# Kernel optimization log

Hardware: AMD Instinct MI355X
Metric: run time of the kernel (lower is better)

## Reference

```python
import jax, jax.numpy as jnp
import numpy as np

D_MODEL = 2048
NUM_HEADS = 16
D_K = 128
SEQ_LEN = 4096
BATCH = 4


def make_rope(max_seq_len, d, dtype=jnp.float32):
    # theta_i = 1/10000^(2i/d), pos_enc = outer(pos, theta), buffer = [sin | cos] along last dim -> [S, d]
    theta = 1.0 / jnp.power(10000.0, jnp.arange(0, d, 2, dtype=dtype) / d)
    pos = jnp.arange(max_seq_len, dtype=dtype)
    pe = pos[:, None] * theta[None, :]                     # [S, d/2]
    return jnp.concatenate([jnp.sin(pe), jnp.cos(pe)], axis=-1)  # [S, d]


def apply_rope(x, rope):
    # x: [..., S, d_k], rope: [S, d_k] (already sliced to S)
    d_k = x.shape[-1]
    scale = jnp.sqrt(jnp.asarray(d_k, dtype=x.dtype))
    x = x * scale
    x1, x2 = x[..., ::2], x[..., 1::2]
    r1, r2 = rope[..., ::2], rope[..., 1::2]
    return jnp.concatenate([x1 * r1 - x2 * r2, x2 * r1 + x1 * r2], axis=-1)


def setup_inputs() -> dict:
    key = jax.random.key(0)
    ks = jax.random.split(key, 7)
    sq = 1.0 / np.sqrt(D_MODEL)
    x = jax.random.normal(ks[0], (BATCH, SEQ_LEN, D_MODEL), dtype=jnp.float32)
    Wq = jax.random.uniform(ks[1], (D_MODEL, NUM_HEADS * D_K), jnp.float32, -sq, sq)
    bq = jax.random.uniform(ks[2], (NUM_HEADS * D_K,), jnp.float32, -sq, sq)
    Wk = jax.random.uniform(ks[3], (D_MODEL, D_K), jnp.float32, -sq, sq)
    bk = jax.random.uniform(ks[4], (D_K,), jnp.float32, -sq, sq)
    Wv = jax.random.uniform(ks[5], (D_MODEL, D_K), jnp.float32, -sq, sq)
    bv = jax.random.uniform(ks[6], (D_K,), jnp.float32, -sq, sq)
    return {"x": x, "Wq": Wq, "bq": bq, "Wk": Wk, "bk": bk, "Wv": Wv, "bv": bv}


def reference(x, Wq, bq, Wk, bk, Wv, bv):
    B, S, _ = x.shape
    rope = make_rope(SEQ_LEN, D_K, x.dtype)[:S]            # [S, d_k]
    Q = (jnp.einsum('bsd,de->bse', x, Wq) + bq)            # [B, S, H*d_k]
    Q = Q.reshape(B, S, NUM_HEADS, D_K).transpose(0, 2, 1, 3)  # [B, H, S, d_k]
    Q = apply_rope(Q, rope)
    K = apply_rope(jnp.einsum('bsd,de->bse', x, Wk) + bk, rope)  # [B, S, d_k]
    V = apply_rope(jnp.einsum('bsd,de->bse', x, Wv) + bv, rope)  # [B, S, d_k]
    return (Q, K, V)
```

## Files before the change

kernel.cpp:

```cpp
#include <hip/hip_runtime.h>
#include <hip/hip_bf16.h>
#include <math.h>

#define D_MODEL 2048
#define NUM_HEADS 16
#define D_K 128
#define SEQ_LEN 4096
#define BATCH 4
#define M_ROWS 16384
#define N_TOT 2304
#define KT 32

#define XB_BYTES 67108864ull
#define WT_BYTES 9437184ull
#define BP_BYTES 16384ull

typedef __attribute__((ext_vector_type(8))) short bf16x8;
typedef __attribute__((ext_vector_type(8))) unsigned short u16x8;
typedef __attribute__((ext_vector_type(4))) float f32x4;

__device__ __forceinline__ unsigned short f2bf(float f) {
  unsigned int u = __builtin_bit_cast(unsigned int, f);
  u += 0x7fffu + ((u >> 16) & 1u);
  return (unsigned short)(u >> 16);
}

__device__ __forceinline__ void async16(const unsigned char* g, unsigned char* l) {
  __builtin_amdgcn_global_load_lds(
      (const __attribute__((address_space(1))) void*)g,
      (__attribute__((address_space(3))) void*)l, 16, 0, 0);
}

__global__ void rope_kernel(float* __restrict__ ropeT) {
  int idx = blockIdx.x * 256 + threadIdx.x;
  int o = idx & 63;
  int sp = idx >> 6;
  int j1 = (o < 32) ? (2 * o) : (2 * (o - 32));
  float th1 = 1.0f / powf(10000.0f, (float)j1 / 64.0f);
  float th2 = 1.0f / powf(10000.0f, (float)(j1 + 1) / 64.0f);
  float a1 = (float)sp * th1;
  float a2 = (float)sp * th2;
  float v1 = (o < 32) ? sinf(a1) : cosf(a1);
  float v2 = (o < 32) ? sinf(a2) : cosf(a2);
  const float sc = 11.3137084989847604f;
  ropeT[sp * 128 + o]      = v1 * sc;
  ropeT[sp * 128 + 64 + o] = v2 * sc;
}

__global__ void bias_kernel(const float* __restrict__ bq, const float* __restrict__ bk,
                            const float* __restrict__ bv, float* __restrict__ bp) {
  int n = blockIdx.x * 256 + threadIdx.x;
  if (n >= N_TOT) return;
  int r = n & 127, nb = n >> 7;
  int d = (r < 64) ? (2 * r) : (2 * (r - 64) + 1);
  float v;
  if (nb < 16)       v = bq[nb * 128 + d];
  else if (nb == 16) v = bk[d];
  else               v = bv[d];
  bp[n] = v;
}

__global__ void wsplit_kernel(const float* __restrict__ Wq, const float* __restrict__ Wk,
                              const float* __restrict__ Wv, unsigned char* __restrict__ wt) {
  int R = threadIdx.x;
  int c   = blockIdx.x & 7;
  int kt  = (blockIdx.x >> 3) & 31;
  int nb2 = blockIdx.x >> 8;
  int wng = R >> 6, q = R & 63, a = q >> 4, lr = q & 15;
  int s = wng >> 1, w = wng & 1;
  int tq = 2 * w + (a & 1) + 4 * (a >> 1);
  int col = tq * 16 + lr;
  int d = (col < 64) ? (2 * col) : (2 * (col - 64) + 1);
  int n = (nb2 * 2 + s) * 128 + d;
  const float* src; int ld, cc;
  if (n < 2048)      { src = Wq; ld = 2048; cc = n; }
  else if (n < 2176) { src = Wk; ld = 128;  cc = n - 2048; }
  else               { src = Wv; ld = 128;  cc = n - 2176; }
  int k0 = kt * 64 + c * 8;
  u16x8 H;
#pragma unroll
  for (int j = 0; j < 8; j++) H[j] = f2bf(src[(size_t)(k0 + j) * ld + cc]);
  unsigned char* tile = wt + (((size_t)(nb2 * 32 + kt)) << 15);
  *(u16x8*)(tile + R * 128 + ((c ^ (R & 7)) << 4)) = H;
}

__global__ void xcast_kernel(const float* __restrict__ x, unsigned char* __restrict__ xb) {
  int idx = blockIdx.x * 256 + threadIdx.x;
  int c  = idx & 7;
  int r  = (idx >> 3) & 255;
  int kt = (idx >> 11) & 31;
  int mb = idx >> 16;
  const float4* p = (const float4*)(x + ((size_t)(mb * 256 + r)) * D_MODEL + kt * 64 + c * 8);
  float4 v0 = p[0], v1 = p[1];
  float v[8] = {v0.x, v0.y, v0.z, v0.w, v1.x, v1.y, v1.z, v1.w};
  u16x8 H;
#pragma unroll
  for (int j = 0; j < 8; j++) H[j] = f2bf(v[j]);
  unsigned char* tile = xb + (((size_t)(mb * 32 + kt)) << 15);
  *(u16x8*)(tile + r * 128 + ((c ^ (r & 7)) << 4)) = H;
}

__global__ __launch_bounds__(512, 2)
void gemm_rope_kernel(const unsigned char* __restrict__ xb,
                      const unsigned char* __restrict__ wt,
                      const float* __restrict__ bp,
                      const float* __restrict__ ropeT,
                      float* __restrict__ out) {
  __shared__ __align__(16) unsigned char lds[131072];

  const int tid = threadIdx.x;
  const int wave = tid >> 6, lane = tid & 63;
  const int lr = lane & 15, gl = lane >> 4;
  const int wm = wave >> 2;
  const int wng = wave & 3;

  int bid = blockIdx.x;
  int wg = (bid & 7) * 72 + (bid >> 3);
  const int mb  = wg / 9;
  const int nb2 = wg % 9;

  const int sw = lr & 7;
  int aoff[8], boff[4];
#pragma unroll
  for (int i = 0; i < 8; i++)
    aoff[i] = (wm * 128 + i * 16 + lr) * 128 + ((gl ^ sw) << 4);
#pragma unroll
  for (int a = 0; a < 4; a++)
    boff[a] = 32768 + (wng * 64 + a * 16 + lr) * 128 + ((gl ^ sw) << 4);

  f32x4 acc[8][4];
#pragma unroll
  for (int i = 0; i < 8; i++)
#pragma unroll
    for (int a = 0; a < 4; a++) acc[i][a] = (f32x4){0.f, 0.f, 0.f, 0.f};

  const unsigned char* gA = xb + ((size_t)(mb * KT) << 15);
  const unsigned char* gB = wt + ((size_t)(nb2 * KT) << 15);
  const int aro = wm * 16384 + wng * 1024;
  const int bro = wng * 8192 + wm * 4096;

#pragma unroll
  for (int j = 0; j < 4; j++)
    async16(gB + bro + j * 1024 + lane * 16, lds + 32768 + bro + j * 1024);
#pragma unroll
  for (int j = 0; j < 4; j++)
    async16(gA + aro + j * 4096 + lane * 16, lds + aro + j * 4096);
  asm volatile("s_waitcnt vmcnt(3)" ::: "memory");
  __builtin_amdgcn_s_barrier();
  __builtin_amdgcn_sched_barrier(0);

#define PHASE_BODY(p, CS, STAGE, K)                                                        \
  {                                                                                        \
    bf16x8 x0h = *(const bf16x8*)(lds + (CS) + aoff[2*(p)]);                               \
    bf16x8 x0l = *(const bf16x8*)(lds + (CS) + (aoff[2*(p)] ^ 64));                        \
    bf16x8 x1h = *(const bf16x8*)(lds + (CS) + aoff[2*(p)+1]);                             \
    bf16x8 x1l = *(const bf16x8*)(lds + (CS) + (aoff[2*(p)+1] ^ 64));                      \
    STAGE                                                                                  \
    __builtin_amdgcn_s_setprio(1);                                                         \
    _Pragma("unroll")                                                                      \
    for (int a_ = 0; a_ < 4; ++a_) {                                                       \
      acc[2*(p)][a_]   = __builtin_amdgcn_mfma_f32_16x16x32_bf16(x0h, bh[a_], acc[2*(p)][a_], 0,0,0);   \
      acc[2*(p)][a_]   = __builtin_amdgcn_mfma_f32_16x16x32_bf16(x0l, bl[a_], acc[2*(p)][a_], 0,0,0);   \
      acc[2*(p)+1][a_] = __builtin_amdgcn_mfma_f32_16x16x32_bf16(x1h, bh[a_], acc[2*(p)+1][a_], 0,0,0); \
      acc[2*(p)+1][a_] = __builtin_amdgcn_mfma_f32_16x16x32_bf16(x1l, bl[a_], acc[2*(p)+1][a_], 0,0,0); \
    }                                                                                      \
    __builtin_amdgcn_s_setprio(0);                                                         \
    asm volatile("s_waitcnt vmcnt(" K ")" ::: "memory");                                   \
    __builtin_amdgcn_s_barrier();                                                          \
    __builtin_amdgcn_sched_barrier(0);                                                     \
  }

#define STAGE_B01 { async16(gBn + bro + lane*16, lB + bro);                 \
                    async16(gBn + bro + 1024 + lane*16, lB + bro + 1024); }
#define STAGE_B23 { async16(gBn + bro + 2048 + lane*16, lB + bro + 2048);   \
                    async16(gBn + bro + 3072 + lane*16, lB + bro + 3072); }
#define STAGE_A01 { async16(gAn + aro + lane*16, lA + aro);                 \
                    async16(gAn + aro + 4096 + lane*16, lA + aro + 4096); }
#define STAGE_A23 { async16(gAn + aro + 8192 + lane*16, lA + aro + 8192);   \
                    async16(gAn + aro + 12288 + lane*16, lA + aro + 12288); }
#define STAGE_NONE {}

  for (int t = 0; t < KT - 1; ++t) {
    const int CS = (t & 1) << 16;
    unsigned char* lA = lds + (CS ^ 65536);
    unsigned char* lB = lA + 32768;
    const unsigned char* gAn = gA + ((size_t)(t + 1) << 15);
    const unsigned char* gBn = gB + ((size_t)(t + 1) << 15);
    bf16x8 bh[4], bl[4];
#pragma unroll
    for (int a = 0; a < 4; a++) {
      bh[a] = *(const bf16x8*)(lds + CS + boff[a]);
      bl[a] = *(const bf16x8*)(lds + CS + (boff[a] ^ 64));
    }
    PHASE_BODY(0, CS, STAGE_B01, "4")
    PHASE_BODY(1, CS, STAGE_B23, "5")
    PHASE_BODY(2, CS, STAGE_A01, "6")
    PHASE_BODY(3, CS, STAGE_A23, "3")
  }
  {
    const int CS = ((KT - 1) & 1) << 16;
    bf16x8 bh[4], bl[4];
#pragma unroll
    for (int a = 0; a < 4; a++) {
      bh[a] = *(const bf16x8*)(lds + CS + boff[a]);
      bl[a] = *(const bf16x8*)(lds + CS + (boff[a] ^ 64));
    }
    PHASE_BODY(0, CS, STAGE_NONE, "2")
    PHASE_BODY(1, CS, STAGE_NONE, "1")
    PHASE_BODY(2, CS, STAGE_NONE, "0")
    PHASE_BODY(3, CS, STAGE_NONE, "0")
  }
#undef PHASE_BODY
#undef STAGE_B01
#undef STAGE_B23
#undef STAGE_A01
#undef STAGE_A23
#undef STAGE_NONE

  const int m0 = mb * 256 + wm * 128;
  const int ssub = wng >> 1, w = wng & 1;
  const int nbv = nb2 * 2 + ssub;
#pragma unroll
  for (int i = 0; i < 8; i++) {
#pragma unroll
    for (int a = 0; a < 2; a++) {
      int op = (2 * w + a) * 16 + lr;
      int nlo = nbv * 128 + op;
      float blo = bp[nlo], bhi = bp[nlo + 64];
#pragma unroll
      for (int r = 0; r < 4; r++) {
        int row = m0 + i * 16 + gl * 4 + r;
        int sp = row & (SEQ_LEN - 1);
        int b = row >> 12;
        float t1 = acc[i][a][r]     + blo;
        float t2 = acc[i][a + 2][r] + bhi;
        float R1 = ropeT[sp * 128 + op];
        float R2 = ropeT[sp * 128 + 64 + op];
        float olo = R1 * t1 - R2 * t2;
        float ohi = R2 * t1 + R1 * t2;
        size_t base;
        if (nbv < 16)       base = (((size_t)(b * NUM_HEADS + nbv)) * SEQ_LEN + sp) * D_K;
        else if (nbv == 16) base = (size_t)M_ROWS * D_MODEL
                                   + ((size_t)(b * SEQ_LEN + sp)) * D_K;
        else                base = (size_t)M_ROWS * D_MODEL + (size_t)M_ROWS * D_K
                                   + ((size_t)(b * SEQ_LEN + sp)) * D_K;
        out[base + op]      = olo;
        out[base + op + 64] = ohi;
      }
    }
  }
}

extern "C" void kernel_launch(void* const* d_in, const int* in_sizes, int n_in,
                              void* d_out, int out_size, void* d_ws, size_t ws_size,
                              hipStream_t stream) {
  const float* x  = (const float*)d_in[0];
  const float* Wq = (const float*)d_in[1];
  const float* bq = (const float*)d_in[2];
  const float* Wk = (const float*)d_in[3];
  const float* bk = (const float*)d_in[4];
  const float* Wv = (const float*)d_in[5];
  const float* bv = (const float*)d_in[6];
  float* out = (float*)d_out;

  unsigned char* ws = (unsigned char*)d_ws;
  unsigned char* xb = ws;
  unsigned char* wt = ws + XB_BYTES;
  float* bp    = (float*)(ws + XB_BYTES + WT_BYTES);
  float* ropeT = (float*)(ws + XB_BYTES + WT_BYTES + BP_BYTES);

  rope_kernel<<<1024, 256, 0, stream>>>(ropeT);
  bias_kernel<<<9, 256, 0, stream>>>(bq, bk, bv, bp);
  wsplit_kernel<<<2304, 256, 0, stream>>>(Wq, Wk, Wv, wt);
  xcast_kernel<<<16384, 256, 0, stream>>>(x, xb);
  gemm_rope_kernel<<<576, 512, 0, stream>>>(xb, wt, bp, ropeT, out);
}
```

Measured before the change: 446.2 us.

## Switch GEMM to 32x32x16 MFMA tiles with simpler per-K-step double buffering

Replaces the 16x16x32 MFMA inner loop with 32x32x16 bf16 MFMAs, rearranging the weight pre-pack layout, the LDS fragment offsets and the epilogue row mapping to match. The fine-grained four-phase staged prefetch with partial vmcnt waits is replaced by issuing the whole next K-tile at the start of each iteration, followed by one full wait and barrier. Larger MFMA tiles cut the number of LDS fragment reads and MFMA issues per FLOP. The coarser synchronization may expose more load latency than the previous interleaved schedule.

```diff
diff --git a/kernel.cpp b/kernel.cpp
--- a/kernel.cpp
+++ b/kernel.cpp
@@ -17,7 +17,7 @@
 
 typedef __attribute__((ext_vector_type(8))) short bf16x8;
 typedef __attribute__((ext_vector_type(8))) unsigned short u16x8;
-typedef __attribute__((ext_vector_type(4))) float f32x4;
+typedef __attribute__((ext_vector_type(16))) float f32x16;
 
 __device__ __forceinline__ unsigned short f2bf(float f) {
   unsigned int u = __builtin_bit_cast(unsigned int, f);
@@ -66,11 +66,10 @@
   int c   = blockIdx.x & 7;
   int kt  = (blockIdx.x >> 3) & 31;
   int nb2 = blockIdx.x >> 8;
-  int wng = R >> 6, q = R & 63, a = q >> 4, lr = q & 15;
-  int s = wng >> 1, w = wng & 1;
-  int tq = 2 * w + (a & 1) + 4 * (a >> 1);
-  int col = tq * 16 + lr;
-  int d = (col < 64) ? (2 * col) : (2 * (col - 64) + 1);
+  int wng = R >> 6, j = (R >> 5) & 1, c31 = R & 31;
+  int opfull = (wng & 1) * 32 + j * 64 + c31;
+  int s = wng >> 1;
+  int d = (opfull < 64) ? (2 * opfull) : (2 * (opfull - 64) + 1);
   int n = (nb2 * 2 + s) * 128 + d;
   const float* src; int ld, cc;
   if (n < 2048)      { src = Wq; ld = 2048; cc = n; }
@@ -79,7 +78,7 @@
   int k0 = kt * 64 + c * 8;
   u16x8 H;
 #pragma unroll
-  for (int j = 0; j < 8; j++) H[j] = f2bf(src[(size_t)(k0 + j) * ld + cc]);
+  for (int jj = 0; jj < 8; jj++) H[jj] = f2bf(src[(size_t)(k0 + jj) * ld + cc]);
   unsigned char* tile = wt + (((size_t)(nb2 * 32 + kt)) << 15);
   *(u16x8*)(tile + R * 128 + ((c ^ (R & 7)) << 4)) = H;
 }
@@ -95,7 +94,7 @@
   float v[8] = {v0.x, v0.y, v0.z, v0.w, v1.x, v1.y, v1.z, v1.w};
   u16x8 H;
 #pragma unroll
-  for (int j = 0; j < 8; j++) H[j] = f2bf(v[j]);
+  for (int jj = 0; jj < 8; jj++) H[jj] = f2bf(v[jj]);
   unsigned char* tile = xb + (((size_t)(mb * 32 + kt)) << 15);
   *(u16x8*)(tile + r * 128 + ((c ^ (r & 7)) << 4)) = H;
 }
@@ -110,7 +109,7 @@
 
   const int tid = threadIdx.x;
   const int wave = tid >> 6, lane = tid & 63;
-  const int lr = lane & 15, gl = lane >> 4;
+  const int c31 = lane & 31, h = lane >> 5;
   const int wm = wave >> 2;
   const int wng = wave & 3;
 
@@ -119,134 +118,111 @@
   const int mb  = wg / 9;
   const int nb2 = wg % 9;
 
-  const int sw = lr & 7;
-  int aoff[8], boff[4];
-#pragma unroll
-  for (int i = 0; i < 8; i++)
-    aoff[i] = (wm * 128 + i * 16 + lr) * 128 + ((gl ^ sw) << 4);
-#pragma unroll
-  for (int a = 0; a < 4; a++)
-    boff[a] = 32768 + (wng * 64 + a * 16 + lr) * 128 + ((gl ^ sw) << 4);
-
-  f32x4 acc[8][4];
-#pragma unroll
-  for (int i = 0; i < 8; i++)
-#pragma unroll
-    for (int a = 0; a < 4; a++) acc[i][a] = (f32x4){0.f, 0.f, 0.f, 0.f};
+  int aoff[4][4], boff[2][4];
+#pragma unroll
+  for (int i = 0; i < 4; i++) {
+    int row = wm * 128 + i * 32 + c31;
+#pragma unroll
+    for (int q = 0; q < 4; q++)
+      aoff[i][q] = row * 128 + (((2 * q + h) ^ (row & 7)) << 4);
+  }
+#pragma unroll
+  for (int j = 0; j < 2; j++) {
+    int rowb = wng * 64 + j * 32 + c31;
+#pragma unroll
+    for (int q = 0; q < 4; q++)
+      boff[j][q] = 32768 + rowb * 128 + (((2 * q + h) ^ (rowb & 7)) << 4);
+  }
+
+  f32x16 acc[4][2];
+#pragma unroll
+  for (int i = 0; i < 4; i++)
+#pragma unroll
+    for (int j = 0; j < 2; j++)
+#pragma unroll
+      for (int r = 0; r < 16; r++) acc[i][j][r] = 0.f;
 
   const unsigned char* gA = xb + ((size_t)(mb * KT) << 15);
   const unsigned char* gB = wt + ((size_t)(nb2 * KT) << 15);
   const int aro = wm * 16384 + wng * 1024;
   const int bro = wng * 8192 + wm * 4096;
 
-#pragma unroll
-  for (int j = 0; j < 4; j++)
-    async16(gB + bro + j * 1024 + lane * 16, lds + 32768 + bro + j * 1024);
-#pragma unroll
-  for (int j = 0; j < 4; j++)
-    async16(gA + aro + j * 4096 + lane * 16, lds + aro + j * 4096);
-  asm volatile("s_waitcnt vmcnt(3)" ::: "memory");
+#define ISSUE(tt)                                                              \
+  do {                                                                         \
+    const unsigned char* gA_ = gA + ((size_t)(tt) << 15) + aro + lane * 16;    \
+    const unsigned char* gB_ = gB + ((size_t)(tt) << 15) + bro + lane * 16;    \
+    unsigned char* lA_ = lds + (((tt) & 1) << 16) + aro;                       \
+    unsigned char* lB_ = lds + (((tt) & 1) << 16) + 32768 + bro;               \
+    async16(gA_,         lA_);                                                 \
+    async16(gA_ + 4096,  lA_ + 4096);                                          \
+    async16(gA_ + 8192,  lA_ + 8192);                                          \
+    async16(gA_ + 12288, lA_ + 12288);                                         \
+    async16(gB_,         lB_);                                                 \
+    async16(gB_ + 1024,  lB_ + 1024);                                          \
+    async16(gB_ + 2048,  lB_ + 2048);                                          \
+    async16(gB_ + 3072,  lB_ + 3072);                                          \
+  } while (0)
+
+  ISSUE(0);
+  asm volatile("s_waitcnt vmcnt(0)" ::: "memory");
   __builtin_amdgcn_s_barrier();
   __builtin_amdgcn_sched_barrier(0);
 
-#define PHASE_BODY(p, CS, STAGE, K)                                                        \
-  {                                                                                        \
-    bf16x8 x0h = *(const bf16x8*)(lds + (CS) + aoff[2*(p)]);                               \
-    bf16x8 x0l = *(const bf16x8*)(lds + (CS) + (aoff[2*(p)] ^ 64));                        \
-    bf16x8 x1h = *(const bf16x8*)(lds + (CS) + aoff[2*(p)+1]);                             \
-    bf16x8 x1l = *(const bf16x8*)(lds + (CS) + (aoff[2*(p)+1] ^ 64));                      \
-    STAGE                                                                                  \
-    __builtin_amdgcn_s_setprio(1);                                                         \
-    _Pragma("unroll")                                                                      \
-    for (int a_ = 0; a_ < 4; ++a_) {                                                       \
-      acc[2*(p)][a_]   = __builtin_amdgcn_mfma_f32_16x16x32_bf16(x0h, bh[a_], acc[2*(p)][a_], 0,0,0);   \
-      acc[2*(p)][a_]   = __builtin_amdgcn_mfma_f32_16x16x32_bf16(x0l, bl[a_], acc[2*(p)][a_], 0,0,0);   \
-      acc[2*(p)+1][a_] = __builtin_amdgcn_mfma_f32_16x16x32_bf16(x1h, bh[a_], acc[2*(p)+1][a_], 0,0,0); \
-      acc[2*(p)+1][a_] = __builtin_amdgcn_mfma_f32_16x16x32_bf16(x1l, bl[a_], acc[2*(p)+1][a_], 0,0,0); \
-    }                                                                                      \
-    __builtin_amdgcn_s_setprio(0);                                                         \
-    asm volatile("s_waitcnt vmcnt(" K ")" ::: "memory");                                   \
-    __builtin_amdgcn_s_barrier();                                                          \
-    __builtin_amdgcn_sched_barrier(0);                                                     \
-  }
-
-#define STAGE_B01 { async16(gBn + bro + lane*16, lB + bro);                 \
-                    async16(gBn + bro + 1024 + lane*16, lB + bro + 1024); }
-#define STAGE_B23 { async16(gBn + bro + 2048 + lane*16, lB + bro + 2048);   \
-                    async16(gBn + bro + 3072 + lane*16, lB + bro + 3072); }
-#define STAGE_A01 { async16(gAn + aro + lane*16, lA + aro);                 \
-                    async16(gAn + aro + 4096 + lane*16, lA + aro + 4096); }
-#define STAGE_A23 { async16(gAn + aro + 8192 + lane*16, lA + aro + 8192);   \
-                    async16(gAn + aro + 12288 + lane*16, lA + aro + 12288); }
-#define STAGE_NONE {}
-
-  for (int t = 0; t < KT - 1; ++t) {
-    const int CS = (t & 1) << 16;
-    unsigned char* lA = lds + (CS ^ 65536);
-    unsigned char* lB = lA + 32768;
-    const unsigned char* gAn = gA + ((size_t)(t + 1) << 15);
-    const unsigned char* gBn = gB + ((size_t)(t + 1) << 15);
-    bf16x8 bh[4], bl[4];
-#pragma unroll
-    for (int a = 0; a < 4; a++) {
-      bh[a] = *(const bf16x8*)(lds + CS + boff[a]);
-      bl[a] = *(const bf16x8*)(lds + CS + (boff[a] ^ 64));
+  for (int t = 0; t < KT; ++t) {
+    if (t + 1 < KT) ISSUE(t + 1);
+    const unsigned char* sl = lds + ((t & 1) << 16);
+#pragma unroll
+    for (int q = 0; q < 4; ++q) {
+      bf16x8 A0 = *(const bf16x8*)(sl + aoff[0][q]);
+      bf16x8 A1 = *(const bf16x8*)(sl + aoff[1][q]);
+      bf16x8 A2 = *(const bf16x8*)(sl + aoff[2][q]);
+      bf16x8 A3 = *(const bf16x8*)(sl + aoff[3][q]);
+      bf16x8 B0 = *(const bf16x8*)(sl + boff[0][q]);
+      bf16x8 B1 = *(const bf16x8*)(sl + boff[1][q]);
+      __builtin_amdgcn_s_setprio(1);
+      acc[0][0] = __builtin_amdgcn_mfma_f32_32x32x16_bf16(A0, B0, acc[0][0], 0, 0, 0);
+      acc[0][1] = __builtin_amdgcn_mfma_f32_32x32x16_bf16(A0, B1, acc[0][1], 0, 0, 0);
+      acc[1][0] = __builtin_amdgcn_mfma_f32_32x32x16_bf16(A1, B0, acc[1][0], 0, 0, 0);
+      acc[1][1] = __builtin_amdgcn_mfma_f32_32x32x16_bf16(A1, B1, acc[1][1], 0, 0, 0);
+      acc[2][0] = __builtin_amdgcn_mfma_f32_32x32x16_bf16(A2, B0, acc[2][0], 0, 0, 0);
+      acc[2][1] = __builtin_amdgcn_mfma_f32_32x32x16_bf16(A2, B1, acc[2][1], 0, 0, 0);
+      acc[3][0] = __builtin_amdgcn_mfma_f32_32x32x16_bf16(A3, B0, acc[3][0], 0, 0, 0);
+      acc[3][1] = __builtin_amdgcn_mfma_f32_32x32x16_bf16(A3, B1, acc[3][1], 0, 0, 0);
+      __builtin_amdgcn_s_setprio(0);
     }
-    PHASE_BODY(0, CS, STAGE_B01, "4")
-    PHASE_BODY(1, CS, STAGE_B23, "5")
-    PHASE_BODY(2, CS, STAGE_A01, "6")
-    PHASE_BODY(3, CS, STAGE_A23, "3")
-  }
-  {
-    const int CS = ((KT - 1) & 1) << 16;
-    bf16x8 bh[4], bl[4];
-#pragma unroll
-    for (int a = 0; a < 4; a++) {
-      bh[a] = *(const bf16x8*)(lds + CS + boff[a]);
-      bl[a] = *(const bf16x8*)(lds + CS + (boff[a] ^ 64));
-    }
-    PHASE_BODY(0, CS, STAGE_NONE, "2")
-    PHASE_BODY(1, CS, STAGE_NONE, "1")
-    PHASE_BODY(2, CS, STAGE_NONE, "0")
-    PHASE_BODY(3, CS, STAGE_NONE, "0")
-  }
-#undef PHASE_BODY
-#undef STAGE_B01
-#undef STAGE_B23
-#undef STAGE_A01
-#undef STAGE_A23
-#undef STAGE_NONE
+    __builtin_amdgcn_sched_barrier(0);
+    asm volatile("s_waitcnt vmcnt(0)" ::: "memory");
+    __builtin_amdgcn_s_barrier();
+    __builtin_amdgcn_sched_barrier(0);
+  }
+#undef ISSUE
 
   const int m0 = mb * 256 + wm * 128;
-  const int ssub = wng >> 1, w = wng & 1;
-  const int nbv = nb2 * 2 + ssub;
-#pragma unroll
-  for (int i = 0; i < 8; i++) {
-#pragma unroll
-    for (int a = 0; a < 2; a++) {
-      int op = (2 * w + a) * 16 + lr;
-      int nlo = nbv * 128 + op;
-      float blo = bp[nlo], bhi = bp[nlo + 64];
-#pragma unroll
-      for (int r = 0; r < 4; r++) {
-        int row = m0 + i * 16 + gl * 4 + r;
-        int sp = row & (SEQ_LEN - 1);
-        int b = row >> 12;
-        float t1 = acc[i][a][r]     + blo;
-        float t2 = acc[i][a + 2][r] + bhi;
-        float R1 = ropeT[sp * 128 + op];
-        float R2 = ropeT[sp * 128 + 64 + op];
-        float olo = R1 * t1 - R2 * t2;
-        float ohi = R2 * t1 + R1 * t2;
-        size_t base;
-        if (nbv < 16)       base = (((size_t)(b * NUM_HEADS + nbv)) * SEQ_LEN + sp) * D_K;
-        else if (nbv == 16) base = (size_t)M_ROWS * D_MODEL
-                                   + ((size_t)(b * SEQ_LEN + sp)) * D_K;
-        else                base = (size_t)M_ROWS * D_MODEL + (size_t)M_ROWS * D_K
-                                   + ((size_t)(b * SEQ_LEN + sp)) * D_K;
-        out[base + op]      = olo;
-        out[base + op + 64] = ohi;
-      }
+  const int op = (wng & 1) * 32 + c31;
+  const int nbv = nb2 * 2 + (wng >> 1);
+  const int nlo = nbv * 128 + op;
+  const float blo = bp[nlo], bhi = bp[nlo + 64];
+#pragma unroll
+  for (int i = 0; i < 4; i++) {
+#pragma unroll
+    for (int r = 0; r < 16; r++) {
+      int row = m0 + i * 32 + 4 * h + (r & 3) + 8 * (r >> 2);
+      int sp = row & (SEQ_LEN - 1);
+      int b = row >> 12;
+      float t1 = acc[i][0][r] + blo;
+      float t2 = acc[i][1][r] + bhi;
+      float R1 = ropeT[sp * 128 + op];
+      float R2 = ropeT[sp * 128 + 64 + op];
+      float olo = R1 * t1 - R2 * t2;
+      float ohi = R2 * t1 + R1 * t2;
+      size_t base;
+      if (nbv < 16)       base = (((size_t)(b * NUM_HEADS + nbv)) * SEQ_LEN + sp) * D_K;
+      else if (nbv == 16) base = (size_t)M_ROWS * D_MODEL
+                                 + ((size_t)(b * SEQ_LEN + sp)) * D_K;
+      else                base = (size_t)M_ROWS * D_MODEL + (size_t)M_ROWS * D_K
+                                 + ((size_t)(b * SEQ_LEN + sp)) * D_K;
+      out[base + op]      = olo;
+      out[base + op + 64] = ohi;
     }
   }
 }
```

Result: slower. 476.4 us (+6.8%).
